# Kernel optimization log

Measured on AMD Instinct MI355X. Metric: run time of the kernel, lower is better.

The kernel has to match this reference:

```python
import jax, jax.numpy as jnp
import numpy as np

N_NODES = 100000
N_EDGES = 1600000
FEAT_DIM = 64
IN_DIM = FEAT_DIM + 3  # feat + xyz


def setup_inputs() -> dict:
    key = jax.random.key(0)
    k1, k2, k3, k4, k5 = jax.random.split(key, 5)
    xyz = jax.random.normal(k1, (N_NODES, 3), dtype=jnp.float32)
    feat = jax.random.normal(k2, (N_NODES, FEAT_DIM), dtype=jnp.float32)
    edge_index = jax.random.randint(k3, (2, N_EDGES), 0, N_NODES, dtype=jnp.int64)
    # MLP params (Linear stored as [in, out] for x @ W + b)
    W1 = jax.random.normal(k4, (2 * IN_DIM, FEAT_DIM), dtype=jnp.float32) * (1.0 / np.sqrt(2 * IN_DIM))
    b1 = jnp.zeros((FEAT_DIM,), dtype=jnp.float32)
    W2 = jax.random.normal(k5, (FEAT_DIM, FEAT_DIM), dtype=jnp.float32) * (1.0 / np.sqrt(FEAT_DIM))
    b2 = jnp.zeros((FEAT_DIM,), dtype=jnp.float32)
    return {"xyz": xyz, "feat": feat, "edge_index": edge_index,
            "W1": W1, "b1": b1, "W2": W2, "b2": b2}


def reference(xyz, feat, edge_index, W1, b1, W2, b2):
    # node features: cat([feat, xyz]) -> [N, C+3]
    x = jnp.concatenate([feat, xyz], axis=-1)
    src = edge_index[0]  # j (source / neighbor)
    dst = edge_index[1]  # i (target, aggregation index)
    x_i = x[dst]                       # [E, C+3]
    x_j = x[src]                       # [E, C+3]
    # EdgeConv message: mlp(cat([x_i, x_j - x_i]))
    m = jnp.concatenate([x_i, x_j - x_i], axis=-1)   # [E, 2*(C+3)]
    h = jax.nn.relu(m @ W1 + b1) @ W2 + b2           # [E, C]
    n = x.shape[0]
    agg = jax.ops.segment_max(h, dst, num_segments=n)  # [N, C]
    # nodes with no incoming edges get 0 (matches PyG scatter-max fill)
    deg = jax.ops.segment_sum(jnp.ones((dst.shape[0],), h.dtype), dst, num_segments=n)
    return jnp.where(deg[:, None] > 0, agg, jnp.zeros_like(agg))
```

## Files before the change

kernel.cpp:

```cpp
#include <hip/hip_runtime.h>
#include <stdint.h>

#define N_NODES 100000
#define FEAT 64
#define NB 64
#define SC_CHUNK 8192
#define NBKT 1563
#define BKT_CAP 1400
#define RVN 6
#define BIAS 512.0f

typedef __attribute__((ext_vector_type(8))) _Float16 half8;
typedef __attribute__((ext_vector_type(2))) _Float16 half2v;
typedef __attribute__((ext_vector_type(2))) __fp16 fp16x2;
typedef __attribute__((ext_vector_type(4))) float f32x4;

__device__ __forceinline__ uint32_t enc_key(float f) {
    uint32_t u = __float_as_uint(f);
    return (u & 0x80000000u) ? ~u : (u | 0x80000000u);
}
__device__ __forceinline__ float dec_key(uint32_t k) {
    return __uint_as_float((k & 0x80000000u) ? (k & 0x7FFFFFFFu) : ~k);
}
__device__ __forceinline__ uint32_t pk_f16(float a, float b) {
    union { fp16x2 h; uint32_t u; } cv;
    cv.h = __builtin_amdgcn_cvt_pkrtz(a, b);
    return cv.u;
}

#define W2T_OFF 0
#define AMB_OFF 4096
#define BM_OFF  8384
#define W2P_OFF 12672
#define U_OFF   16384
#define V_OFF   (U_OFF + N_NODES * FEAT / 2)
#define GCNT_OFF (U_OFF + N_NODES * FEAT)
#define SRT_OFF  (GCNT_OFF + 2048)

__global__ __launch_bounds__(256) void transform_kernel(
    const float* __restrict__ W1, const float* __restrict__ W2,
    float* __restrict__ ws, int full)
{
    int i = blockIdx.x * 256 + threadIdx.x;
    if (full && i < 2048)
        ((uint32_t*)ws)[GCNT_OFF + i] = 0u;
    if (i < 4096) {
        int c2 = i >> 6, c = i & 63;
        ws[W2T_OFF + i] = W2[c * 64 + c2];
    } else if (full && i < 8384) {
        int j = i - 4096;
        ws[AMB_OFF + j] = W1[j] - W1[j + 67 * 64];
    } else if (full && i < 12672) {
        int j = i - 8384;
        ws[BM_OFF + j] = W1[j + 67 * 64];
    } else if (full && i < 16768) {
        int p = i - 12672;
        int j = p & 7, c2lo = (p >> 3) & 15, quad = (p >> 7) & 3;
        int h = (p >> 9) & 1, n4 = (p >> 10) & 3;
        int k = h * 32 + quad * 8 + j;
        int n = n4 * 16 + c2lo;
        ((_Float16*)(ws + W2P_OFF))[p] = (_Float16)W2[k * 64 + n];
    }
}

__global__ __launch_bounds__(256) void nodebkt_kernel(
    const float* __restrict__ xyz, const float* __restrict__ feat,
    const float* __restrict__ b1, const float* __restrict__ ws,
    uint16_t* __restrict__ U, uint16_t* __restrict__ V, int nN,
    const int* __restrict__ ei, uint32_t* __restrict__ gcnt,
    uint32_t* __restrict__ sorted, int nE, int nBkt)
{
    __shared__ uint32_t svals[SC_CHUNK];
    __shared__ uint16_t sbkt[SC_CHUNK];
    __shared__ uint32_t hist[NBKT];
    __shared__ uint32_t base[NBKT + 1];
    __shared__ uint32_t segs[256];

    int t = threadIdx.x;

    if ((int)blockIdx.x < nBkt) {
        int e0 = blockIdx.x * SC_CHUNK;
        int cnt = min(SC_CHUNK, nE - e0);
        int cnt4 = cnt & ~3;

        for (int i = t; i < NBKT; i += 256) hist[i] = 0;
        __syncthreads();
        for (int i = t * 4; i < cnt4; i += 1024) {
            uint4 d4 = *(const uint4*)(ei + nE + e0 + i);
            atomicAdd(&hist[d4.x >> 6], 1u);
            atomicAdd(&hist[d4.y >> 6], 1u);
            atomicAdd(&hist[d4.z >> 6], 1u);
            atomicAdd(&hist[d4.w >> 6], 1u);
        }
        for (int i = cnt4 + t; i < cnt; i += 256)
            atomicAdd(&hist[ei[nE + e0 + i] >> 6], 1u);
        __syncthreads();
        {
            const int SEG = 7;
            int lo = t * SEG, hi = min(lo + SEG, NBKT);
            uint32_t s = 0;
            for (int i = lo; i < hi; ++i) s += hist[i];
            segs[t] = s;
            __syncthreads();
            for (int d = 1; d < 256; d <<= 1) {
                uint32_t x = (t >= d) ? segs[t - d] : 0;
                __syncthreads();
                segs[t] += x;
                __syncthreads();
            }
            uint32_t run = (t == 0) ? 0 : segs[t - 1];
            for (int i = lo; i < hi; ++i) { uint32_t c = hist[i]; base[i] = run; run += c; }
            if (t == 255) base[NBKT] = run;
        }
        __syncthreads();
        for (int i = t; i < NBKT; i += 256) hist[i] = base[i];
        __syncthreads();
        for (int i = t * 4; i < cnt4; i += 1024) {
            uint4 s4 = *(const uint4*)(ei + e0 + i);
            uint4 d4 = *(const uint4*)(ei + nE + e0 + i);
            uint32_t sa[4] = {(uint32_t)s4.x, (uint32_t)s4.y, (uint32_t)s4.z, (uint32_t)s4.w};
            uint32_t da[4] = {(uint32_t)d4.x, (uint32_t)d4.y, (uint32_t)d4.z, (uint32_t)d4.w};
            #pragma unroll
            for (int k = 0; k < 4; ++k) {
                uint32_t b = da[k] >> 6;
                uint32_t pos = atomicAdd(&hist[b], 1u);
                svals[pos] = sa[k] | ((da[k] & 63u) << 20);
                sbkt[pos] = (uint16_t)b;
            }
        }
        for (int i = cnt4 + t; i < cnt; i += 256) {
            uint32_t src = (uint32_t)ei[e0 + i];
            uint32_t dst = (uint32_t)ei[nE + e0 + i];
            uint32_t b = dst >> 6;
            uint32_t pos = atomicAdd(&hist[b], 1u);
            svals[pos] = src | ((dst & 63u) << 20);
            sbkt[pos] = (uint16_t)b;
        }
        __syncthreads();
        for (int b = t; b < NBKT; b += 256) {
            uint32_t c = base[b + 1] - base[b];
            hist[b] = c ? atomicAdd(&gcnt[b], c) : 0u;
        }
        __syncthreads();
        for (int i = t * 4; i < cnt4; i += 1024) {
            ushort4 b4 = *(const ushort4*)(sbkt + i);
            uint4 v4 = *(const uint4*)(svals + i);
            uint32_t ba[4] = {b4.x, b4.y, b4.z, b4.w};
            uint32_t va[4] = {v4.x, v4.y, v4.z, v4.w};
            #pragma unroll
            for (int k = 0; k < 4; ++k) {
                uint32_t b = ba[k];
                uint32_t off = hist[b] + ((uint32_t)(i + k) - base[b]);
                if (off < BKT_CAP)
                    sorted[(size_t)b * BKT_CAP + off] = va[k];
            }
        }
        for (int i = cnt4 + t; i < cnt; i += 256) {
            uint32_t b = sbkt[i];
            uint32_t off = hist[b] + ((uint32_t)i - base[b]);
            if (off < BKT_CAP)
                sorted[(size_t)b * BKT_CAP + off] = svals[i];
        }
        return;
    }

    int nb = blockIdx.x - nBkt;
    int half = nb & 1;
    int n = (nb >> 1) * 256 + t;
    if (n >= nN) return;
    const float* __restrict__ W = ws + (half ? BM_OFF : AMB_OFF);

    float acc[FEAT];
    if (half == 0) {
        #pragma unroll
        for (int c = 0; c < FEAT; ++c) acc[c] = b1[c];
    } else {
        #pragma unroll
        for (int c = 0; c < FEAT; ++c) acc[c] = 0.0f;
    }

    const float* f = feat + (size_t)n * FEAT;
    #pragma unroll 1
    for (int k = 0; k < 64; k += 4) {
        float4 x4 = *(const float4*)(f + k);
        float xv[4] = {x4.x, x4.y, x4.z, x4.w};
        #pragma unroll
        for (int q = 0; q < 4; ++q) {
            const float* __restrict__ w = W + (k + q) * 64;
            #pragma unroll
            for (int c = 0; c < FEAT; ++c)
                acc[c] = fmaf(xv[q], w[c], acc[c]);
        }
    }
    const float* p = xyz + (size_t)n * 3;
    #pragma unroll
    for (int k3 = 0; k3 < 3; ++k3) {
        float xv = p[k3];
        const float* __restrict__ w = W + (64 + k3) * 64;
        #pragma unroll
        for (int c = 0; c < FEAT; ++c)
            acc[c] = fmaf(xv, w[c], acc[c]);
    }
    uint4* outp = (uint4*)((half ? V : U) + (size_t)n * FEAT);
    #pragma unroll
    for (int q = 0; q < 8; ++q) {
        uint4 o;
        o.x = pk_f16(acc[8*q + 0], acc[8*q + 1]);
        o.y = pk_f16(acc[8*q + 2], acc[8*q + 3]);
        o.z = pk_f16(acc[8*q + 4], acc[8*q + 5]);
        o.w = pk_f16(acc[8*q + 6], acc[8*q + 7]);
        outp[q] = o;
    }
}

#define LOADE(G, DSV, VV0, VV1, UU0, UU1) do {                               \
        int e_c_ = min((G) + el, cnt - 1);                                   \
        uint32_t val_ = ssrt[e_c_];                                          \
        DSV = *(const uint4*)(ssrt + (G) + quad * 4);                        \
        int src_ = (int)(val_ & 0xFFFFFu);                                   \
        const uint32_t* vr_ = (const uint32_t*)(V + (size_t)src_ * FEAT);    \
        VV0 = *(const uint4*)(vr_ + quad * 4);                               \
        VV1 = *(const uint4*)(vr_ + 16 + quad * 4);                          \
        const uint32_t* ur_ = ushare + (int)(val_ >> 20) * 32;               \
        UU0 = *(const uint4*)(ur_ + quad * 4);                               \
        UU1 = *(const uint4*)(ur_ + 16 + quad * 4);                          \
    } while (0)

__global__ __launch_bounds__(256) void agg_kernel(
    const uint32_t* __restrict__ gcnt, const uint32_t* __restrict__ sorted,
    const uint16_t* __restrict__ U, const uint16_t* __restrict__ V,
    const float* __restrict__ ws_w2p, const float* __restrict__ b2,
    float* __restrict__ out, int nN)
{
    __shared__ int      lmax[NB * 65];
    __shared__ uint32_t ushare[NB * 32];
    __shared__ uint32_t ssrt[BKT_CAP + 16];
    __shared__ uint32_t shist[NB];

    int bkt = blockIdx.x;
    int nb0 = bkt * NB;
    int rows = min(NB, nN - nb0);
    int cnt = min((int)gcnt[bkt], BKT_CAP);
    int t = threadIdx.x;

    for (int i = t; i < NB * 65; i += 256) lmax[i] = 0;
    if (t < NB) shist[t] = 0;
    {
        const uint4* usrc4 = (const uint4*)(U + (size_t)nb0 * FEAT);
        for (int i = t; i < rows * 8; i += 256) ((uint4*)ushare)[i] = usrc4[i];
    }
    const uint32_t* bsrc = sorted + (size_t)bkt * BKT_CAP;
    __syncthreads();

    uint32_t rv[RVN];
    #pragma unroll
    for (int j = 0; j < RVN; ++j) {
        int i = t + j * 256;
        if (i < cnt) {
            uint32_t v = bsrc[i];
            rv[j] = v;
            atomicAdd(&shist[v >> 20], 1u);
        }
    }
    __syncthreads();
    if (t < NB) {
        uint32_t v = shist[t];
        uint32_t run = v;
        #pragma unroll
        for (int d = 1; d < 64; d <<= 1) {
            uint32_t x = (uint32_t)__shfl_up((int)run, (unsigned)d, 64);
            if (t >= d) run += x;
        }
        shist[t] = run - v;
    }
    __syncthreads();
    #pragma unroll
    for (int j = 0; j < RVN; ++j) {
        int i = t + j * 256;
        if (i < cnt) {
            uint32_t v = rv[j];
            uint32_t pos = atomicAdd(&shist[v >> 20], 1u);
            ssrt[pos] = v;
        }
    }
    __syncthreads();

    int lane = t & 63;
    int wave = t >> 6;
    int el = lane & 15, quad = lane >> 4;

    const uint4* w2p = (const uint4*)ws_w2p;
    union { uint4 u4; half8 h8; } bfr[8];
    #pragma unroll
    for (int q8 = 0; q8 < 8; ++q8)
        bfr[q8].u4 = w2p[(q8 * 4 + quad) * 16 + el];
    float b2v[4];
    #pragma unroll
    for (int n4 = 0; n4 < 4; ++n4) b2v[n4] = b2[n4 * 16 + el] + BIAS;

    const half2v zero2 = {(_Float16)0.0f, (_Float16)0.0f};

    uint4 dsv_c, vv_c0, vv_c1, uu_c0, uu_c1;
    int g = wave * 16;
    if (g < cnt) LOADE(g, dsv_c, vv_c0, vv_c1, uu_c0, uu_c1);

    #pragma unroll 1
    for (; g < cnt; g += 64) {
        int gn = g + 64;
        int gl = (gn < cnt) ? gn : g;
        uint4 dsv_n, vv_n0, vv_n1, uu_n0, uu_n1;
        LOADE(gl, dsv_n, vv_n0, vv_n1, uu_n0, uu_n1);

        union { uint4 u4; half8 h8; } afr[2];
        #pragma unroll
        for (int h = 0; h < 2; ++h) {
            uint4 uu = h ? uu_c1 : uu_c0;
            uint4 vv = h ? vv_c1 : vv_c0;
            uint32_t ua[4] = {uu.x, uu.y, uu.z, uu.w};
            uint32_t va[4] = {vv.x, vv.y, vv.z, vv.w};
            uint32_t pk[4];
            #pragma unroll
            for (int p = 0; p < 4; ++p) {
                union { uint32_t u; half2v h2; } cu, cv2, ct;
                cu.u = ua[p]; cv2.u = va[p];
                ct.h2 = __builtin_elementwise_max(cu.h2 + cv2.h2, zero2);
                pk[p] = ct.u;
            }
            afr[h].u4 = make_uint4(pk[0], pk[1], pk[2], pk[3]);
        }

        f32x4 acc[4];
        #pragma unroll
        for (int n4 = 0; n4 < 4; ++n4)
            acc[n4] = (f32x4){b2v[n4], b2v[n4], b2v[n4], b2v[n4]};
        #pragma unroll
        for (int n4 = 0; n4 < 4; ++n4) {
            acc[n4] = __builtin_amdgcn_mfma_f32_16x16x32_f16(afr[0].h8, bfr[n4*2+0].h8, acc[n4], 0, 0, 0);
            acc[n4] = __builtin_amdgcn_mfma_f32_16x16x32_f16(afr[1].h8, bfr[n4*2+1].h8, acc[n4], 0, 0, 0);
        }

        int d0 = (int)(dsv_c.x >> 20), d1 = (int)(dsv_c.y >> 20);
        int d2 = (int)(dsv_c.z >> 20), d3 = (int)(dsv_c.w >> 20);
        int eb = g + quad * 4;
        bool ok0 = eb < cnt, ok1 = eb + 1 < cnt;
        bool ok2 = eb + 2 < cnt, ok3 = eb + 3 < cnt;
        bool m0 = (d0 == d1) & ok1;
        bool m1 = (d1 == d2) & ok2;
        bool m2 = (d2 == d3) & ok3;
        #pragma unroll
        for (int n4 = 0; n4 < 4; ++n4) {
            if (m0) acc[n4][1] = fmaxf(acc[n4][1], acc[n4][0]);
            if (m1) acc[n4][2] = fmaxf(acc[n4][2], acc[n4][1]);
            if (m2) acc[n4][3] = fmaxf(acc[n4][3], acc[n4][2]);
        }
        if (ok0 & !m0) {
            #pragma unroll
            for (int n4 = 0; n4 < 4; ++n4)
                atomicMax(&lmax[d0 * 65 + n4 * 16 + el], __float_as_int(acc[n4][0]));
        }
        if (ok1 & !m1) {
            #pragma unroll
            for (int n4 = 0; n4 < 4; ++n4)
                atomicMax(&lmax[d1 * 65 + n4 * 16 + el], __float_as_int(acc[n4][1]));
        }
        if (ok2 & !m2) {
            #pragma unroll
            for (int n4 = 0; n4 < 4; ++n4)
                atomicMax(&lmax[d2 * 65 + n4 * 16 + el], __float_as_int(acc[n4][2]));
        }
        if (ok3) {
            #pragma unroll
            for (int n4 = 0; n4 < 4; ++n4)
                atomicMax(&lmax[d3 * 65 + n4 * 16 + el], __float_as_int(acc[n4][3]));
        }

        dsv_c = dsv_n;
        vv_c0 = vv_n0; vv_c1 = vv_n1;
        uu_c0 = uu_n0; uu_c1 = uu_n1;
    }
    __syncthreads();

    for (int i = t * 4; i < rows * FEAT; i += 1024) {
        int r = i >> 6, c = i & 63;
        int lb = r * 65 + c;
        int k0 = lmax[lb + 0], k1 = lmax[lb + 1];
        int k2 = lmax[lb + 2], k3 = lmax[lb + 3];
        float4 o;
        o.x = k0 ? (__int_as_float(k0) - BIAS) : 0.0f;
        o.y = k1 ? (__int_as_float(k1) - BIAS) : 0.0f;
        o.z = k2 ? (__int_as_float(k2) - BIAS) : 0.0f;
        o.w = k3 ? (__int_as_float(k3) - BIAS) : 0.0f;
        *(float4*)(out + (size_t)(nb0 + r) * FEAT + c) = o;
    }
}
#undef LOADE

__device__ __forceinline__ void rank1_update(
    float* __restrict__ h, float xi, float d,
    const float* __restrict__ A, const float* __restrict__ B)
{
    #pragma unroll
    for (int c = 0; c < FEAT; ++c)
        h[c] = fmaf(xi, A[c], fmaf(d, B[c], h[c]));
}

__global__ __launch_bounds__(256) void edge_fused_kernel(
    const float* __restrict__ xyz, const float* __restrict__ feat,
    const int* __restrict__ ei,
    const float* __restrict__ W1, const float* __restrict__ b1,
    const float* __restrict__ ws, const float* __restrict__ b2,
    uint32_t* __restrict__ keys, int nE)
{
    int e = blockIdx.x * 256 + threadIdx.x;
    if (e >= nE) return;
    int src = ei[e];
    int dst = ei[nE + e];
    const float* __restrict__ W2T = ws + W2T_OFF;

    float h[FEAT];
    #pragma unroll
    for (int c = 0; c < FEAT; ++c) h[c] = b1[c];

    const float* fi = feat + (size_t)dst * FEAT;
    const float* fj = feat + (size_t)src * FEAT;
    #pragma unroll 1
    for (int k = 0; k < 64; k += 4) {
        float4 a = *(const float4*)(fi + k);
        float4 b = *(const float4*)(fj + k);
        rank1_update(h, a.x, b.x - a.x, W1 + (k + 0) * 64, W1 + (67 + k + 0) * 64);
        rank1_update(h, a.y, b.y - a.y, W1 + (k + 1) * 64, W1 + (67 + k + 1) * 64);
        rank1_update(h, a.z, b.z - a.z, W1 + (k + 2) * 64, W1 + (67 + k + 2) * 64);
        rank1_update(h, a.w, b.w - a.w, W1 + (k + 3) * 64, W1 + (67 + k + 3) * 64);
    }
    {
        const float* pi = xyz + (size_t)dst * 3;
        const float* pj = xyz + (size_t)src * 3;
        #pragma unroll
        for (int k3 = 0; k3 < 3; ++k3) {
            float xi = pi[k3];
            rank1_update(h, xi, pj[k3] - xi, W1 + (64 + k3) * 64, W1 + (131 + k3) * 64);
        }
    }
    #pragma unroll
    for (int c = 0; c < FEAT; ++c) h[c] = fmaxf(h[c], 0.0f);

    uint32_t* krow = keys + (size_t)dst * FEAT;
    #pragma unroll 1
    for (int c2 = 0; c2 < FEAT; c2 += 4) {
        float o0 = b2[c2 + 0], o1 = b2[c2 + 1];
        float o2 = b2[c2 + 2], o3 = b2[c2 + 3];
        const float* w0 = W2T + (c2 + 0) * 64;
        const float* w1 = W2T + (c2 + 1) * 64;
        const float* w2 = W2T + (c2 + 2) * 64;
        const float* w3 = W2T + (c2 + 3) * 64;
        #pragma unroll
        for (int c = 0; c < FEAT; ++c) {
            float hv = h[c];
            o0 = fmaf(hv, w0[c], o0);
            o1 = fmaf(hv, w1[c], o1);
            o2 = fmaf(hv, w2[c], o2);
            o3 = fmaf(hv, w3[c], o3);
        }
        uint32_t k0 = enc_key(o0), k1 = enc_key(o1);
        uint32_t k2 = enc_key(o2), k3 = enc_key(o3);
        uint4 cur = *(const uint4*)(krow + c2);
        if (k0 > cur.x) atomicMax(&krow[c2 + 0], k0);
        if (k1 > cur.y) atomicMax(&krow[c2 + 1], k1);
        if (k2 > cur.z) atomicMax(&krow[c2 + 2], k2);
        if (k3 > cur.w) atomicMax(&krow[c2 + 3], k3);
    }
}

__global__ __launch_bounds__(256) void decode_kernel(
    uint32_t* __restrict__ keys, int n4)
{
    int i = blockIdx.x * 256 + threadIdx.x;
    if (i >= n4) return;
    uint4 k = ((const uint4*)keys)[i];
    float4 r;
    r.x = k.x ? dec_key(k.x) : 0.0f;
    r.y = k.y ? dec_key(k.y) : 0.0f;
    r.z = k.z ? dec_key(k.z) : 0.0f;
    r.w = k.w ? dec_key(k.w) : 0.0f;
    ((float4*)keys)[i] = r;
}

extern "C" void kernel_launch(void* const* d_in, const int* in_sizes, int n_in,
                              void* d_out, int out_size, void* d_ws, size_t ws_size,
                              hipStream_t stream)
{
    const float* xyz  = (const float*)d_in[0];
    const float* feat = (const float*)d_in[1];
    const int*   ei   = (const int*)d_in[2];
    const float* W1   = (const float*)d_in[3];
    const float* b1   = (const float*)d_in[4];
    const float* W2   = (const float*)d_in[5];
    const float* b2   = (const float*)d_in[6];

    int nE = in_sizes[2] / 2;
    float* ws = (float*)d_ws;

    size_t need_words = (size_t)SRT_OFF + (size_t)NBKT * BKT_CAP;
    int full = (ws_size >= need_words * 4) ? 1 : 0;

    transform_kernel<<<66, 256, 0, stream>>>(W1, W2, ws, full);

    if (full) {
        uint16_t* U = (uint16_t*)(ws + U_OFF);
        uint16_t* V = (uint16_t*)(ws + V_OFF);
        uint32_t* gcnt   = (uint32_t*)(ws + GCNT_OFF);
        uint32_t* sorted = (uint32_t*)(ws + SRT_OFF);

        int nBkt = (nE + SC_CHUNK - 1) / SC_CHUNK;
        int nodeBlocks = ((N_NODES + 255) / 256) * 2;
        nodebkt_kernel<<<nBkt + nodeBlocks, 256, 0, stream>>>(
            xyz, feat, b1, ws, U, V, N_NODES, ei, gcnt, sorted, nE, nBkt);
        agg_kernel<<<NBKT, 256, 0, stream>>>(
            gcnt, sorted, U, V, ws + W2P_OFF, b2, (float*)d_out, N_NODES);
    } else {
        uint32_t* keys = (uint32_t*)d_out;
        hipMemsetAsync(d_out, 0, (size_t)out_size * sizeof(float), stream);
        edge_fused_kernel<<<(nE + 255) / 256, 256, 0, stream>>>(
            xyz, feat, ei, W1, b1, ws, b2, keys, nE);
        decode_kernel<<<(out_size / 4 + 255) / 256, 256, 0, stream>>>(
            keys, out_size / 4);
    }
}
```

Baseline: 175.0 us.

## Scatter edges directly to global buckets, dropping shared-memory local sort

The bucketing phase no longer does a block-local prefix scan and a staged reorder through shared memory. Each block now reserves global bucket offsets right after building its histogram, then writes each edge straight to its global slot using a shared atomic cursor. This removes the scan, the extra passes and roughly 50KB of LDS, which should raise occupancy, but the global writes become scattered rather than grouped by bucket.

```diff
diff --git a/kernel.cpp b/kernel.cpp
--- a/kernel.cpp
+++ b/kernel.cpp
@@ -70,11 +70,7 @@
     const int* __restrict__ ei, uint32_t* __restrict__ gcnt,
     uint32_t* __restrict__ sorted, int nE, int nBkt)
 {
-    __shared__ uint32_t svals[SC_CHUNK];
-    __shared__ uint16_t sbkt[SC_CHUNK];
     __shared__ uint32_t hist[NBKT];
-    __shared__ uint32_t base[NBKT + 1];
-    __shared__ uint32_t segs[256];
 
     int t = threadIdx.x;
 
@@ -95,25 +91,10 @@
         for (int i = cnt4 + t; i < cnt; i += 256)
             atomicAdd(&hist[ei[nE + e0 + i] >> 6], 1u);
         __syncthreads();
-        {
-            const int SEG = 7;
-            int lo = t * SEG, hi = min(lo + SEG, NBKT);
-            uint32_t s = 0;
-            for (int i = lo; i < hi; ++i) s += hist[i];
-            segs[t] = s;
-            __syncthreads();
-            for (int d = 1; d < 256; d <<= 1) {
-                uint32_t x = (t >= d) ? segs[t - d] : 0;
-                __syncthreads();
-                segs[t] += x;
-                __syncthreads();
-            }
-            uint32_t run = (t == 0) ? 0 : segs[t - 1];
-            for (int i = lo; i < hi; ++i) { uint32_t c = hist[i]; base[i] = run; run += c; }
-            if (t == 255) base[NBKT] = run;
-        }
-        __syncthreads();
-        for (int i = t; i < NBKT; i += 256) hist[i] = base[i];
+        for (int b = t; b < NBKT; b += 256) {
+            uint32_t c = hist[b];
+            hist[b] = c ? atomicAdd(&gcnt[b], c) : 0u;
+        }
         __syncthreads();
         for (int i = t * 4; i < cnt4; i += 1024) {
             uint4 s4 = *(const uint4*)(ei + e0 + i);
@@ -124,8 +105,8 @@
             for (int k = 0; k < 4; ++k) {
                 uint32_t b = da[k] >> 6;
                 uint32_t pos = atomicAdd(&hist[b], 1u);
-                svals[pos] = sa[k] | ((da[k] & 63u) << 20);
-                sbkt[pos] = (uint16_t)b;
+                if (pos < BKT_CAP)
+                    sorted[(size_t)b * BKT_CAP + pos] = sa[k] | ((da[k] & 63u) << 20);
             }
         }
         for (int i = cnt4 + t; i < cnt; i += 256) {
@@ -133,33 +114,8 @@
             uint32_t dst = (uint32_t)ei[nE + e0 + i];
             uint32_t b = dst >> 6;
             uint32_t pos = atomicAdd(&hist[b], 1u);
-            svals[pos] = src | ((dst & 63u) << 20);
-            sbkt[pos] = (uint16_t)b;
-        }
-        __syncthreads();
-        for (int b = t; b < NBKT; b += 256) {
-            uint32_t c = base[b + 1] - base[b];
-            hist[b] = c ? atomicAdd(&gcnt[b], c) : 0u;
-        }
-        __syncthreads();
-        for (int i = t * 4; i < cnt4; i += 1024) {
-            ushort4 b4 = *(const ushort4*)(sbkt + i);
-            uint4 v4 = *(const uint4*)(svals + i);
-            uint32_t ba[4] = {b4.x, b4.y, b4.z, b4.w};
-            uint32_t va[4] = {v4.x, v4.y, v4.z, v4.w};
-            #pragma unroll
-            for (int k = 0; k < 4; ++k) {
-                uint32_t b = ba[k];
-                uint32_t off = hist[b] + ((uint32_t)(i + k) - base[b]);
-                if (off < BKT_CAP)
-                    sorted[(size_t)b * BKT_CAP + off] = va[k];
-            }
-        }
-        for (int i = cnt4 + t; i < cnt; i += 256) {
-            uint32_t b = sbkt[i];
-            uint32_t off = hist[b] + ((uint32_t)i - base[b]);
-            if (off < BKT_CAP)
-                sorted[(size_t)b * BKT_CAP + off] = svals[i];
+            if (pos < BKT_CAP)
+                sorted[(size_t)b * BKT_CAP + pos] = src | ((dst & 63u) << 20);
         }
         return;
     }
```

New measurement: 189.4 us. 8.2% more time.
